# Kernel optimization log

Measured on AMD Instinct MI355X. Metric: run time of the kernel, lower is better.

Reference implementation:

```python
import jax, jax.numpy as jnp
import numpy as np
import math

B, L, D = 2, 2048, 768
H, DK = 8, 64
DV = D // H  # 96
N_POS = 32
DFF = 2 * D
EPS = 1e-5


def setup_inputs() -> dict:
    key = jax.random.key(0)
    ks = jax.random.split(key, 12)
    s = 0.02
    return {
        "x": jax.random.normal(ks[0], (B, L, D), jnp.float32),
        "norm1_w": jnp.ones((D,), jnp.float32),
        "norm2_w": jnp.ones((D,), jnp.float32),
        "wq": jax.random.normal(ks[1], (D, H * DK), jnp.float32) * s,
        "wk": jax.random.normal(ks[2], (D, H * DK), jnp.float32) * s,
        "wv": jax.random.normal(ks[3], (D, H * DV), jnp.float32) * s,
        "wo": jax.random.normal(ks[4], (H * DV, D), jnp.float32) * s,
        "bo": jnp.zeros((D,), jnp.float32),
        "u_param": jax.random.normal(ks[5], (H, DK), jnp.float32) * s,
        "v_param": jax.random.normal(ks[6], (H, DK), jnp.float32) * s,
        "w_pos": jax.random.normal(ks[7], (H, DK, N_POS), jnp.float32) * s,
        "w1": jax.random.normal(ks[8], (D, DFF), jnp.float32) * s,
        "b1": jnp.zeros((DFF,), jnp.float32),
        "w2": jax.random.normal(ks[9], (DFF, D), jnp.float32) * s,
        "b2": jnp.zeros((D,), jnp.float32),
    }


def _rel_basis(l: int, n: int) -> jnp.ndarray:
    # Enformer-style central-mask relative position basis: [l, l, n]
    pos = jnp.arange(l)
    distance = pos[None, :] - pos[:, None]  # [l, l]
    pow_rate = jnp.exp(jnp.log(jnp.float32((l + 1) / 2.0)) / (n // 2))
    center_widths = pow_rate ** jnp.arange(1, n // 2 + 1, dtype=jnp.float32)
    d = distance[:, :, None].astype(jnp.float32)
    unsigned = (jnp.abs(d) <= center_widths).astype(jnp.float32)
    signed = jnp.sign(d) * unsigned
    return jnp.concatenate([unsigned, signed], axis=-1)  # [l, l, n]


def _rmsnorm(x, w):
    norm = jnp.mean(x * x, axis=-1, keepdims=True)
    return x * jax.lax.rsqrt(norm + EPS) * w


def reference(x, norm1_w, norm2_w, wq, wk, wv, wo, bo,
              u_param, v_param, w_pos, w1, b1, w2, b2):
    b, l, _ = x.shape
    skip = x
    h1 = _rmsnorm(x, norm1_w)

    q = (h1 @ wq).reshape(b, l, H, DK)
    k = (h1 @ wk).reshape(b, l, H, DK)
    v = (h1 @ wv).reshape(b, l, H, DV)

    basis = _rel_basis(l, N_POS)  # [l, l, n]
    scale = 1.0 / math.sqrt(DK)

    # qr_term: contract q with w_pos first, then with basis (avoids [h,l,l,d] r)
    qw = jnp.einsum('bihd,hdn->bihn', q, w_pos)          # [b,l,h,n]
    qr = jnp.einsum('bihn,ijn->bhij', qw, basis)          # [b,h,l,l]
    uk = jnp.einsum('hd,bjhd->bhj', u_param, k)[:, :, None, :]  # [b,h,1,l]
    vw = jnp.einsum('hd,hdn->hn', v_param, w_pos)         # [h,n]
    vr = jnp.einsum('hn,ijn->hij', vw, basis)[None]       # [1,h,l,l]

    bias = (qr + uk + vr) * scale
    scores = jnp.einsum('bihd,bjhd->bhij', q, k) * scale + bias
    attn = jax.nn.softmax(scores, axis=-1)
    out = jnp.einsum('bhij,bjhd->bihd', attn, v)          # [b,l,h,dv]

    out = out.reshape(b, l, H * DV) @ wo + bo
    x = out + skip

    skip = x
    h2 = _rmsnorm(x, norm2_w)
    h2 = jax.nn.gelu(h2 @ w1 + b1, approximate=False) @ w2 + b2
    return h2 + skip
```

## Files before the change

kernel.cpp:

```cpp
#include <hip/hip_runtime.h>

#define B_ 2
#define L_ 2048
#define D_ 768
#define H_ 8
#define DK_ 64
#define DV_ 96
#define NPOS_ 32

typedef __attribute__((ext_vector_type(8))) __bf16 bf16x8;
typedef __attribute__((ext_vector_type(4))) __bf16 bf16x4;
typedef __attribute__((ext_vector_type(4))) float f32x4;

static __device__ __forceinline__ float bs2f(short s) {
    return (float)__builtin_bit_cast(__bf16, s);
}
static __device__ __forceinline__ short f2bs(float f) {
    return __builtin_bit_cast(short, (__bf16)f);
}

typedef __attribute__((address_space(1))) void gas_void;
typedef __attribute__((address_space(3))) void las_void;
static __device__ __forceinline__ void gload16(const short* g, char* l) {
    __builtin_amdgcn_global_load_lds((const gas_void*)g, (las_void*)l, 16, 0, 0);
}

__global__ __launch_bounds__(256) void prep_kernel(
    const float* __restrict__ wq, const float* __restrict__ wk,
    const float* __restrict__ wv, const float* __restrict__ wo,
    const float* __restrict__ w1, const float* __restrict__ w2,
    const float* __restrict__ vparam, const float* __restrict__ uparam,
    const float* __restrict__ wpos,
    short* __restrict__ wqkvT, short* __restrict__ woT,
    short* __restrict__ w1T, short* __restrict__ w2T,
    unsigned char* __restrict__ sidx, float* __restrict__ VU, float* __restrict__ VS,
    const float* __restrict__ x, const float* __restrict__ n1w, short* __restrict__ h1)
{
    __shared__ short T[64][66];
    __shared__ float vw[H_ * NPOS_];
    __shared__ float uw[H_ * NPOS_];
    __shared__ float red[4];
    int blk = blockIdx.x, tid = threadIdx.x;
    if (blk < 1056) {
        const float* W; short* Wt; int K, N, bx, by;
        if (blk < 96)       { W = wq; Wt = wqkvT;              K = 768;  N = 512;  int b = blk;       bx = b % 8;  by = b / 8; }
        else if (blk < 192) { W = wk; Wt = wqkvT + 512 * 768;  K = 768;  N = 512;  int b = blk - 96;  bx = b % 8;  by = b / 8; }
        else if (blk < 336) { W = wv; Wt = wqkvT + 1024 * 768; K = 768;  N = 768;  int b = blk - 192; bx = b % 12; by = b / 12; }
        else if (blk < 480) { W = wo; Wt = woT;                K = 768;  N = 768;  int b = blk - 336; bx = b % 12; by = b / 12; }
        else if (blk < 768) { W = w1; Wt = w1T;                K = 768;  N = 1536; int b = blk - 480; bx = b % 24; by = b / 24; }
        else                { W = w2; Wt = w2T;                K = 1536; N = 768;  int b = blk - 768; bx = b % 12; by = b / 12; }
        int n0 = bx << 6, k0 = by << 6;
        for (int idx = tid; idx < 4096; idx += 256) {
            int r = idx >> 6, c = idx & 63;
            T[c][r] = f2bs(W[(size_t)(k0 + r) * N + n0 + c]);
        }
        __syncthreads();
        for (int idx = tid; idx < 4096; idx += 256) {
            int r = idx >> 6, c = idx & 63;
            Wt[(size_t)(n0 + r) * K + k0 + c] = T[r][c];
        }
    } else if (blk == 1056) {
        float pr = expf(logf((L_ + 1) / 2.0f) / (NPOS_ / 2));
        for (int idx = tid; idx < 4095; idx += 256) {
            int d = idx - 2047;
            int ad = d < 0 ? -d : d;
            int c = 0;
            for (int m = 1; m <= NPOS_ / 2; ++m) {
                float cw = powf(pr, (float)m);
                if (cw < (float)ad) c++;
            }
            sidx[idx] = (unsigned char)(d > 0 ? c : (d < 0 ? 17 + c : 34));
        }
        {
            int h = tid >> 5, n = tid & 31;
            float av = 0.f, au = 0.f;
            for (int d = 0; d < DK_; ++d) {
                float wp = wpos[(h * DK_ + d) * NPOS_ + n];
                av += vparam[h * DK_ + d] * wp;
                au += uparam[h * DK_ + d] * wp;
            }
            vw[tid] = av;
            uw[tid] = au;
        }
        __syncthreads();
        if (tid < H_ * 17) {
            int h = tid / 17, m = tid % 17;
            float su = 0.f, ss = 0.f;
            for (int t2 = m; t2 < 16; ++t2) {
                su += vw[h * NPOS_ + t2] - uw[h * NPOS_ + t2];
                ss += vw[h * NPOS_ + 16 + t2] - uw[h * NPOS_ + 16 + t2];
            }
            VU[h * 17 + m] = su * 0.125f;
            VS[h * 17 + m] = ss * 0.125f;
        }
    } else {
        int row = blk - 1057;
        const float* xr = x + (size_t)row * D_;
        float ss = 0.f;
        for (int c = tid; c < D_; c += 256) { float f = xr[c]; ss += f * f; }
        for (int msk = 1; msk < 64; msk <<= 1) ss += __shfl_xor(ss, msk);
        if ((tid & 63) == 0) red[tid >> 6] = ss;
        __syncthreads();
        float tot = red[0] + red[1] + red[2] + red[3];
        float sc = rsqrtf(tot * (1.f / D_) + 1e-5f);
        for (int c = tid; c < D_; c += 256)
            h1[(size_t)row * D_ + c] = f2bs(xr[c] * sc * n1w[c]);
    }
}

__global__ __launch_bounds__(256) void rmsnorm_kernel(
    const float* __restrict__ x, const float* __restrict__ wgt, short* __restrict__ out)
{
    int row = blockIdx.x, tid = threadIdx.x;
    __shared__ float red[4];
    const float* xr = x + (size_t)row * D_;
    float ss = 0.f;
    for (int c = tid; c < D_; c += 256) { float f = xr[c]; ss += f * f; }
    for (int msk = 1; msk < 64; msk <<= 1) ss += __shfl_xor(ss, msk);
    if ((tid & 63) == 0) red[tid >> 6] = ss;
    __syncthreads();
    float tot = red[0] + red[1] + red[2] + red[3];
    float sc = rsqrtf(tot * (1.f / D_) + 1e-5f);
    for (int c = tid; c < D_; c += 256)
        out[(size_t)row * D_ + c] = f2bs(xr[c] * sc * wgt[c]);
}

template<int BN>
__global__ __launch_bounds__(512, 4) void gemmx(
    const short* __restrict__ A, const short* __restrict__ Bt,
    const float* __restrict__ bias, const float* __restrict__ uadd,
    const float* __restrict__ resid, void* __restrict__ outp,
    int M, int N, int K, int act, int out_f32)
{
    constexpr int STRIDE = 16384 + BN * 128;
    __shared__ __align__(16) char ldsb[2 * STRIDE];
    int tid = threadIdx.x;
    int w = tid >> 6, lane = tid & 63, quad = lane >> 4, t = lane & 15;
    int wm = (w >> 1) << 5;
    int wn = (w & 1) * (BN / 2);
    int m0b = blockIdx.y << 7, n0b = blockIdx.x * BN;

    int srow = tid >> 3;
    int scol = ((tid & 7) ^ (srow & 7)) << 3;
    const short* aSrc0 = A + (size_t)(m0b + srow) * K + scol;
    const short* aSrc1 = A + (size_t)(m0b + 64 + srow) * K + scol;
    const short* bSrc0 = Bt + (size_t)(n0b + srow) * K + scol;
    const short* bSrc1 = Bt + (size_t)(n0b + 64 + srow) * K + scol;
    int wo1024 = w << 10;

    f32x4 acc[2][BN / 32] = {};

    gload16(aSrc0, ldsb + wo1024);
    gload16(aSrc1, ldsb + 8192 + wo1024);
    gload16(bSrc0, ldsb + 16384 + wo1024);
    if (BN == 128) gload16(bSrc1, ldsb + 16384 + 8192 + wo1024);

    int swz = (t & 7) << 4;
    int cur = 0;
    for (int kb = 0; kb < K; kb += 64) {
        __syncthreads();
        if (kb + 64 < K) {
            char* nb = ldsb + (cur ^ 1) * STRIDE;
            gload16(aSrc0 + kb + 64, nb + wo1024);
            gload16(aSrc1 + kb + 64, nb + 8192 + wo1024);
            gload16(bSrc0 + kb + 64, nb + 16384 + wo1024);
            if (BN == 128) gload16(bSrc1 + kb + 64, nb + 16384 + 8192 + wo1024);
        }
        char* Ab = ldsb + cur * STRIDE;
        char* Bb = Ab + 16384;
#pragma unroll
        for (int ks = 0; ks < 2; ++ks) {
            int cb = ((ks << 6) + (quad << 4)) ^ swz;
            bf16x8 af[2], bf[BN / 32];
#pragma unroll
            for (int ms = 0; ms < 2; ++ms)
                af[ms] = *(const bf16x8*)(Ab + (wm + ms * 16 + t) * 128 + cb);
#pragma unroll
            for (int ns = 0; ns < BN / 32; ++ns)
                bf[ns] = *(const bf16x8*)(Bb + (wn + ns * 16 + t) * 128 + cb);
#pragma unroll
            for (int ms = 0; ms < 2; ++ms)
#pragma unroll
                for (int ns = 0; ns < BN / 32; ++ns)
                    acc[ms][ns] = __builtin_amdgcn_mfma_f32_16x16x32_bf16(af[ms], bf[ns], acc[ms][ns], 0, 0, 0);
        }
        cur ^= 1;
    }
#pragma unroll
    for (int ms = 0; ms < 2; ++ms)
#pragma unroll
        for (int ns = 0; ns < BN / 32; ++ns)
#pragma unroll
            for (int r = 0; r < 4; ++r) {
                int row = m0b + wm + ms * 16 + (quad << 2) + r;
                int col = n0b + wn + ns * 16 + t;
                float v2 = acc[ms][ns][r];
                if (uadd && col < 512) v2 = 0.125f * (v2 + uadd[col]);
                if (bias) v2 += bias[col];
                if (act == 1) v2 = 0.5f * v2 * (1.f + erff(v2 * 0.70710678118654752f));
                if (resid) v2 += resid[(size_t)row * N + col];
                if (out_f32) ((float*)outp)[(size_t)row * N + col] = v2;
                else ((short*)outp)[(size_t)row * N + col] = f2bs(v2);
            }
}

__global__ __launch_bounds__(256) void qv_kernel(
    const short* __restrict__ qkv, const float* __restrict__ wpos,
    const float* __restrict__ VU, const float* __restrict__ VS,
    float* __restrict__ Tg, short* __restrict__ vT, short* __restrict__ kT)
{
    __shared__ __align__(16) char arena[69696];
    int blk = blockIdx.x, tid = threadIdx.x;
    if (blk < 256) {
        float* wl   = (float*)arena;
        float* qrow = (float*)(arena + 65536);
        float* qw   = (float*)(arena + 67584);
        float* sU   = (float*)(arena + 68608);
        float* sS   = (float*)(arena + 69152);
        for (int idx = tid; idx < 4096; idx += 256)
            ((float4*)wl)[idx] = ((const float4*)wpos)[idx];
        int r0 = blk << 4;
        int h = tid >> 5, n = tid & 31;
        for (int rr = 0; rr < 16; ++rr) {
            int row = r0 + rr;
            __syncthreads();
            const short* base = qkv + (size_t)row * 1792;
            qrow[tid]       = bs2f(base[tid]);
            qrow[tid + 256] = bs2f(base[tid + 256]);
            __syncthreads();
            float acc = 0.f;
            for (int d = 0; d < DK_; ++d)
                acc += qrow[h * DK_ + d] * wl[(h * DK_ + d) * 32 + n];
            qw[tid] = acc;
            __syncthreads();
            if (tid < 136) {
                int hh = tid / 17, m = tid % 17;
                float su = 0.f, ss = 0.f;
                for (int t2 = m; t2 < 16; ++t2) { su += qw[hh * NPOS_ + t2]; ss += qw[hh * NPOS_ + 16 + t2]; }
                sU[tid] = su + VU[tid];
                sS[tid] = ss + VS[tid];
            }
            __syncthreads();
            if (tid < 280) {
                int h2 = tid / 35, s = tid % 35;
                int m = s < 17 ? s : (s < 34 ? s - 17 : 0);
                float su = sU[h2 * 17 + m], ss = sS[h2 * 17 + m];
                Tg[(size_t)row * 280 + tid] = s < 17 ? su + ss : (s < 34 ? su - ss : su);
            }
        }
    } else if (blk < 512) {
        short* T = (short*)arena;
        int vb = blk - 256;
        int bh = vb >> 4, b = bh >> 3, h = bh & 7;
        int j0 = (vb & 15) << 7;
#pragma unroll
        for (int it = 0; it < 6; ++it) {
            int idx = tid + (it << 8);
            int row = idx / 12, c8 = (idx % 12) << 3;
            *(bf16x8*)&T[row * 104 + c8] =
                *(const bf16x8*)&qkv[(size_t)(b * L_ + j0 + row) * 1792 + 1024 + h * DV_ + c8];
        }
        __syncthreads();
#pragma unroll
        for (int it = 0; it < 6; ++it) {
            int idx = tid + (it << 8);
            int sub = idx / 768;
            int rem = idx - sub * 768;
            int f = rem >> 6, l = rem & 63;
            int dv = f >> 1, ks = f & 1;
            int q = l >> 4, t = l & 15;
            bf16x8 o;
#pragma unroll
            for (int e = 0; e < 8; ++e) {
                int jl = ((e & 3) << 4) + (ks << 3) + (q << 1) + (e >> 2);
                o[e] = __builtin_bit_cast(__bf16, T[(sub * 64 + jl) * 104 + dv * 16 + t]);
            }
            int jt = ((vb & 15) << 1) + sub;
            *(bf16x8*)&vT[((((size_t)bh * 32 + jt) * 12 + f) * 64 + l) * 8] = o;
        }
    } else {
        short* T = (short*)arena;
        int vb = blk - 512;
        int bh = vb >> 4, b = bh >> 3, h = bh & 7;
        int c128 = vb & 15;
        int j0 = c128 << 7;
#pragma unroll
        for (int it = 0; it < 4; ++it) {
            int idx = tid + (it << 8);
            int row = idx >> 3, c8 = (idx & 7) << 3;
            *(bf16x8*)&T[row * 72 + c8] =
                *(const bf16x8*)&qkv[(size_t)(b * L_ + j0 + row) * 1792 + 512 + h * DK_ + c8];
        }
        __syncthreads();
#pragma unroll
        for (int it = 0; it < 4; ++it) {
            int idx = tid + (it << 8);
            int sub = idx >> 9;
            int rem = idx & 511;
            int f = rem >> 6, l = rem & 63;
            int q = l >> 4, tt = l & 15;
            bf16x8 o = *(bf16x8*)&T[(sub * 64 + (f >> 1) * 16 + tt) * 72 + ((f & 1) << 5) + (q << 3)];
            int jt = (c128 << 1) + sub;
            *(bf16x8*)&kT[((((size_t)bh * 32 + jt) * 8 + f) * 64 + l) * 8] = o;
        }
    }
}

__global__ __launch_bounds__(256, 4) void flash_kernel(
    const short* __restrict__ qkv, const short* __restrict__ kT,
    const short* __restrict__ vT, const float* __restrict__ Tg,
    const unsigned char* __restrict__ sidx_g, short* __restrict__ ao)
{
    __shared__ __align__(16) char arena[17920];
    int tid = threadIdx.x;
    int w = tid >> 6, lane = tid & 63, quad = lane >> 4, t = lane & 15;
    int iw = w >> 1, jg = w & 1;
    short* Pl = (short*)(arena + w * 2304);
    float* Tt = (float*)(arena + 9216);
    unsigned char* sidxl = (unsigned char*)(arena + 13824);

    int id = blockIdx.x;
    int bh8 = id & 7, rest = id >> 3;
    int x = rest & 63, hi = rest >> 6;
    int bh = bh8 + (hi << 3);
    int b = bh >> 3, h = bh & 7;
    int i0 = x << 5;

    for (int idx = tid; idx < 32 * 35; idx += 256) {
        int il = idx / 35, s = idx - il * 35;
        Tt[il * 36 + s] = Tg[(size_t)(b * L_ + i0 + il) * 280 + h * 35 + s];
    }
    for (int idx = tid; idx < 4095; idx += 256) sidxl[idx] = sidx_g[idx];
    __syncthreads();

    int iq = i0 + iw * 16 + t;
    const short* qbase = qkv + (size_t)(b * L_ + iq) * 1792 + h * DK_;
    bf16x8 qf0 = *(const bf16x8*)(qbase + (quad << 3));
    bf16x8 qf1 = *(const bf16x8*)(qbase + 32 + (quad << 3));

    f32x4 O[6] = {};
    float lsum[4] = {0.f, 0.f, 0.f, 0.f};
    const short* kfb = kT + (size_t)bh * 32 * 8 * 512 + lane * 8;
    const short* vfb = vT + (size_t)bh * 32 * 12 * 512 + lane * 8;

    for (int tix = 0; tix < 16; ++tix) {
        int jt = (tix << 1) + jg;
        int j0 = jt << 6;
        bf16x8 kf[8];
#pragma unroll
        for (int f = 0; f < 8; ++f)
            kf[f] = *(const bf16x8*)(kfb + ((size_t)jt * 8 + f) * 512);
        __builtin_amdgcn_sched_barrier(0);

        f32x4 S[4];
        __builtin_amdgcn_s_setprio(1);
#pragma unroll
        for (int ct = 0; ct < 4; ++ct) {
            f32x4 z = {};
            z = __builtin_amdgcn_mfma_f32_16x16x32_bf16(qf0, kf[ct * 2], z, 0, 0, 0);
            S[ct] = __builtin_amdgcn_mfma_f32_16x16x32_bf16(qf1, kf[ct * 2 + 1], z, 0, 0, 0);
        }
        __builtin_amdgcn_s_setprio(0);

        bf16x8 vf[12];
#pragma unroll
        for (int f = 0; f < 12; ++f)
            vf[f] = *(const bf16x8*)(vfb + ((size_t)jt * 12 + f) * 512);
        __builtin_amdgcn_sched_barrier(0);

#pragma unroll
        for (int r = 0; r < 4; ++r) {
            int il = (quad << 2) + r;
            int i = i0 + iw * 16 + il;
            const float* Trow = &Tt[(iw * 16 + il) * 36];
            bf16x4 pv;
#pragma unroll
            for (int ct = 0; ct < 4; ++ct) {
                int j = j0 + ct * 16 + t;
                int s = sidxl[j - i + 2047];
                float p = __expf(S[ct][r] + Trow[s]);
                __bf16 pb = (__bf16)p;
                pv[ct] = pb;
                lsum[r] += (float)pb;
            }
            *(bf16x4*)&Pl[il * 72 + t * 4] = pv;
        }
        __builtin_amdgcn_s_setprio(1);
#pragma unroll
        for (int ks = 0; ks < 2; ++ks) {
            bf16x8 pa = *(bf16x8*)&Pl[t * 72 + (ks << 5) + (quad << 3)];
#pragma unroll
            for (int dv = 0; dv < 6; ++dv)
                O[dv] = __builtin_amdgcn_mfma_f32_16x16x32_bf16(pa, vf[dv * 2 + ks], O[dv], 0, 0, 0);
        }
        __builtin_amdgcn_s_setprio(0);
    }

    __syncthreads();
    float* F = (float*)arena;
    int fl = (iw << 6) + lane;
    if (jg == 1) {
#pragma unroll
        for (int dv = 0; dv < 6; ++dv)
#pragma unroll
            for (int r = 0; r < 4; ++r)
                F[((dv << 2) + r) * 128 + fl] = O[dv][r];
#pragma unroll
        for (int r = 0; r < 4; ++r) F[(24 + r) * 128 + fl] = lsum[r];
    }
    __syncthreads();
    if (jg == 0) {
#pragma unroll
        for (int r = 0; r < 4; ++r) {
            float lr = lsum[r] + F[(24 + r) * 128 + fl];
            lr += __shfl_xor(lr, 1);
            lr += __shfl_xor(lr, 2);
            lr += __shfl_xor(lr, 4);
            lr += __shfl_xor(lr, 8);
            float inv = 1.f / lr;
            int i = i0 + iw * 16 + (quad << 2) + r;
            size_t base = (size_t)(b * L_ + i) * D_ + h * DV_;
#pragma unroll
            for (int dv = 0; dv < 6; ++dv)
                ao[base + dv * 16 + t] = f2bs((O[dv][r] + F[((dv << 2) + r) * 128 + fl]) * inv);
        }
    }
}

extern "C" void kernel_launch(void* const* d_in, const int* in_sizes, int n_in,
                              void* d_out, int out_size, void* d_ws, size_t ws_size,
                              hipStream_t stream)
{
    const float* x    = (const float*)d_in[0];
    const float* n1w  = (const float*)d_in[1];
    const float* n2w  = (const float*)d_in[2];
    const float* wq   = (const float*)d_in[3];
    const float* wk   = (const float*)d_in[4];
    const float* wv   = (const float*)d_in[5];
    const float* wo   = (const float*)d_in[6];
    const float* bo   = (const float*)d_in[7];
    const float* up   = (const float*)d_in[8];
    const float* vp   = (const float*)d_in[9];
    const float* wpos = (const float*)d_in[10];
    const float* w1   = (const float*)d_in[11];
    const float* b1   = (const float*)d_in[12];
    const float* w2   = (const float*)d_in[13];
    const float* b2   = (const float*)d_in[14];

    char* ws = (char*)d_ws;
    short* h1   = (short*)(ws + 0);
    short* qkv  = (short*)(ws + 6291456);
    float* Tg   = (float*)(ws + 20971520);
    float* VUg  = (float*)(ws + 25559040);
    float* VSg  = (float*)(ws + 25560064);
    unsigned char* sidx = (unsigned char*)(ws + 25561088);
    short* ao   = (short*)(ws + 25569280);
    float* x2   = (float*)(ws + 31860736);
    short* vT   = (short*)(ws + 31860736);
    short* kT   = (short*)(ws + 38152192);
    short* wqkvT= (short*)(ws + 44443648);
    short* woT  = (short*)(ws + 47196160);
    short* w1T  = (short*)(ws + 48375808);
    short* w2T  = (short*)(ws + 50735104);
    short* f1   = (short*)(ws + 0);
    short* h2n  = (short*)(ws + 14680064);

    prep_kernel<<<5153, 256, 0, stream>>>(wq, wk, wv, wo, w1, w2, vp, up, wpos,
                                          wqkvT, woT, w1T, w2T, sidx, VUg, VSg,
                                          x, n1w, h1);
    gemmx<128><<<dim3(14, 32), 512, 0, stream>>>(h1, wqkvT, nullptr, up, nullptr, qkv, 4096, 1792, 768, 0, 0);
    qv_kernel<<<768, 256, 0, stream>>>(qkv, wpos, VUg, VSg, Tg, vT, kT);
    flash_kernel<<<dim3(1024), 256, 0, stream>>>(qkv, kT, vT, Tg, sidx, ao);
    gemmx<64><<<dim3(12, 32), 512, 0, stream>>>(ao, woT, bo, nullptr, x, x2, 4096, 768, 768, 0, 1);
    rmsnorm_kernel<<<4096, 256, 0, stream>>>(x2, n2w, h2n);
    gemmx<128><<<dim3(12, 32), 512, 0, stream>>>(h2n, w1T, b1, nullptr, nullptr, f1, 4096, 1536, 768, 1, 0);
    gemmx<64><<<dim3(12, 32), 512, 0, stream>>>(f1, w2T, b2, nullptr, x2, d_out, 4096, 768, 1536, 0, 1);
}
```

Before: 286.3 us.

## Split flash attention key range across four waves per 16-row tile

The flash kernel now gives each block 16 query rows instead of 32. All four waves share those rows and each handles a quarter of the key tiles, combining partial outputs through a two-stage LDS reduction. The grid doubles to 2048 blocks and launch bounds rise to 8 blocks per CU, aiming for more parallelism and occupancy. The cost is redoing per-block setup (Tt and sidx loads) in twice as many blocks and extra reduction syncs. Separately, qv_kernel keeps the w_pos column in registers and reads q rows directly as bf16x8 vectors, removing the 64KB LDS staging and two syncthreads per row.

```diff
diff --git a/kernel.cpp b/kernel.cpp
--- a/kernel.cpp
+++ b/kernel.cpp
@@ -212,25 +212,26 @@
     __shared__ __align__(16) char arena[69696];
     int blk = blockIdx.x, tid = threadIdx.x;
     if (blk < 256) {
-        float* wl   = (float*)arena;
-        float* qrow = (float*)(arena + 65536);
-        float* qw   = (float*)(arena + 67584);
-        float* sU   = (float*)(arena + 68608);
-        float* sS   = (float*)(arena + 69152);
-        for (int idx = tid; idx < 4096; idx += 256)
-            ((float4*)wl)[idx] = ((const float4*)wpos)[idx];
+        float* qw = (float*)arena;
+        float* sU = (float*)(arena + 1024);
+        float* sS = (float*)(arena + 1568);
+        int h = tid >> 5, n = tid & 31;
+        float wlr[64];
+#pragma unroll
+        for (int d = 0; d < DK_; ++d)
+            wlr[d] = wpos[(h * DK_ + d) * NPOS_ + n];
         int r0 = blk << 4;
-        int h = tid >> 5, n = tid & 31;
         for (int rr = 0; rr < 16; ++rr) {
             int row = r0 + rr;
-            __syncthreads();
-            const short* base = qkv + (size_t)row * 1792;
-            qrow[tid]       = bs2f(base[tid]);
-            qrow[tid + 256] = bs2f(base[tid + 256]);
-            __syncthreads();
+            const short* base = qkv + (size_t)row * 1792 + h * DK_;
             float acc = 0.f;
-            for (int d = 0; d < DK_; ++d)
-                acc += qrow[h * DK_ + d] * wl[(h * DK_ + d) * 32 + n];
+#pragma unroll
+            for (int c8 = 0; c8 < 8; ++c8) {
+                bf16x8 q8 = *(const bf16x8*)(base + (c8 << 3));
+#pragma unroll
+                for (int e = 0; e < 8; ++e)
+                    acc += (float)q8[e] * wlr[(c8 << 3) + e];
+            }
             qw[tid] = acc;
             __syncthreads();
             if (tid < 136) {
@@ -306,34 +307,33 @@
     }
 }
 
-__global__ __launch_bounds__(256, 4) void flash_kernel(
+__global__ __launch_bounds__(256, 8) void flash_kernel(
     const short* __restrict__ qkv, const short* __restrict__ kT,
     const short* __restrict__ vT, const float* __restrict__ Tg,
     const unsigned char* __restrict__ sidx_g, short* __restrict__ ao)
 {
-    __shared__ __align__(16) char arena[17920];
+    __shared__ __align__(16) char arena[15616];
     int tid = threadIdx.x;
     int w = tid >> 6, lane = tid & 63, quad = lane >> 4, t = lane & 15;
-    int iw = w >> 1, jg = w & 1;
     short* Pl = (short*)(arena + w * 2304);
     float* Tt = (float*)(arena + 9216);
-    unsigned char* sidxl = (unsigned char*)(arena + 13824);
+    unsigned char* sidxl = (unsigned char*)(arena + 11520);
 
     int id = blockIdx.x;
     int bh8 = id & 7, rest = id >> 3;
-    int x = rest & 63, hi = rest >> 6;
+    int x = rest & 127, hi = rest >> 7;
     int bh = bh8 + (hi << 3);
     int b = bh >> 3, h = bh & 7;
-    int i0 = x << 5;
-
-    for (int idx = tid; idx < 32 * 35; idx += 256) {
+    int i0 = x << 4;
+
+    for (int idx = tid; idx < 16 * 35; idx += 256) {
         int il = idx / 35, s = idx - il * 35;
         Tt[il * 36 + s] = Tg[(size_t)(b * L_ + i0 + il) * 280 + h * 35 + s];
     }
     for (int idx = tid; idx < 4095; idx += 256) sidxl[idx] = sidx_g[idx];
     __syncthreads();
 
-    int iq = i0 + iw * 16 + t;
+    int iq = i0 + t;
     const short* qbase = qkv + (size_t)(b * L_ + iq) * 1792 + h * DK_;
     bf16x8 qf0 = *(const bf16x8*)(qbase + (quad << 3));
     bf16x8 qf1 = *(const bf16x8*)(qbase + 32 + (quad << 3));
@@ -343,8 +343,8 @@
     const short* kfb = kT + (size_t)bh * 32 * 8 * 512 + lane * 8;
     const short* vfb = vT + (size_t)bh * 32 * 12 * 512 + lane * 8;
 
-    for (int tix = 0; tix < 16; ++tix) {
-        int jt = (tix << 1) + jg;
+    for (int tix = 0; tix < 8; ++tix) {
+        int jt = (tix << 2) + w;
         int j0 = jt << 6;
         bf16x8 kf[8];
 #pragma unroll
@@ -371,8 +371,8 @@
 #pragma unroll
         for (int r = 0; r < 4; ++r) {
             int il = (quad << 2) + r;
-            int i = i0 + iw * 16 + il;
-            const float* Trow = &Tt[(iw * 16 + il) * 36];
+            int i = i0 + il;
+            const float* Trow = &Tt[il * 36];
             bf16x4 pv;
 #pragma unroll
             for (int ct = 0; ct < 4; ++ct) {
@@ -398,31 +398,54 @@
 
     __syncthreads();
     float* F = (float*)arena;
-    int fl = (iw << 6) + lane;
-    if (jg == 1) {
+    if (w >= 2) {
+        int col = ((w - 2) << 6) + lane;
 #pragma unroll
         for (int dv = 0; dv < 6; ++dv)
 #pragma unroll
             for (int r = 0; r < 4; ++r)
-                F[((dv << 2) + r) * 128 + fl] = O[dv][r];
-#pragma unroll
-        for (int r = 0; r < 4; ++r) F[(24 + r) * 128 + fl] = lsum[r];
+                F[((dv << 2) + r) * 128 + col] = O[dv][r];
+#pragma unroll
+        for (int r = 0; r < 4; ++r) F[(24 + r) * 128 + col] = lsum[r];
     }
     __syncthreads();
-    if (jg == 0) {
+    if (w < 2) {
+        int col = (w << 6) + lane;
+#pragma unroll
+        for (int dv = 0; dv < 6; ++dv)
+#pragma unroll
+            for (int r = 0; r < 4; ++r)
+                O[dv][r] += F[((dv << 2) + r) * 128 + col];
+#pragma unroll
+        for (int r = 0; r < 4; ++r) lsum[r] += F[(24 + r) * 128 + col];
+    }
+    __syncthreads();
+    if (w == 1) {
+        int col = 64 + lane;
+#pragma unroll
+        for (int dv = 0; dv < 6; ++dv)
+#pragma unroll
+            for (int r = 0; r < 4; ++r)
+                F[((dv << 2) + r) * 128 + col] = O[dv][r];
+#pragma unroll
+        for (int r = 0; r < 4; ++r) F[(24 + r) * 128 + col] = lsum[r];
+    }
+    __syncthreads();
+    if (w == 0) {
+        int col = 64 + lane;
 #pragma unroll
         for (int r = 0; r < 4; ++r) {
-            float lr = lsum[r] + F[(24 + r) * 128 + fl];
+            float lr = lsum[r] + F[(24 + r) * 128 + col];
             lr += __shfl_xor(lr, 1);
             lr += __shfl_xor(lr, 2);
             lr += __shfl_xor(lr, 4);
             lr += __shfl_xor(lr, 8);
             float inv = 1.f / lr;
-            int i = i0 + iw * 16 + (quad << 2) + r;
+            int i = i0 + (quad << 2) + r;
             size_t base = (size_t)(b * L_ + i) * D_ + h * DV_;
 #pragma unroll
             for (int dv = 0; dv < 6; ++dv)
-                ao[base + dv * 16 + t] = f2bs((O[dv][r] + F[((dv << 2) + r) * 128 + fl]) * inv);
+                ao[base + dv * 16 + t] = f2bs((O[dv][r] + F[((dv << 2) + r) * 128 + col]) * inv);
         }
     }
 }
@@ -470,7 +493,7 @@
                                           x, n1w, h1);
     gemmx<128><<<dim3(14, 32), 512, 0, stream>>>(h1, wqkvT, nullptr, up, nullptr, qkv, 4096, 1792, 768, 0, 0);
     qv_kernel<<<768, 256, 0, stream>>>(qkv, wpos, VUg, VSg, Tg, vT, kT);
-    flash_kernel<<<dim3(1024), 256, 0, stream>>>(qkv, kT, vT, Tg, sidx, ao);
+    flash_kernel<<<dim3(2048), 256, 0, stream>>>(qkv, kT, vT, Tg, sidx, ao);
     gemmx<64><<<dim3(12, 32), 512, 0, stream>>>(ao, woT, bo, nullptr, x, x2, 4096, 768, 768, 0, 1);
     rmsnorm_kernel<<<4096, 256, 0, stream>>>(x2, n2w, h2n);
     gemmx<128><<<dim3(12, 32), 512, 0, stream>>>(h2n, w1T, b1, nullptr, nullptr, f1, 4096, 1536, 768, 1, 0);
```

New measurement: 548.1 us. 91.5% more time.
